# Optimization experiments

Measured on AMD Instinct MI355X. Metric: run time of the kernel, lower is better.

## Reference

```python
import jax, jax.numpy as jnp
import numpy as np
from jax import lax

SEGMENTS = 64
KERNEL = 5


def setup_inputs() -> dict:
    key = jax.random.key(0)
    k1, k2, k3 = jax.random.split(key, 3)
    B, S, F = 4, 4096, 1024
    A6 = 512 * 6
    inp = jax.random.normal(k1, (B, S, F), dtype=jnp.float32)
    W = jax.random.normal(k2, (A6, F), dtype=jnp.float32) * (1.0 / np.sqrt(F))
    b = jax.random.normal(k3, (A6,), dtype=jnp.float32) * 0.01
    return {"inp": inp, "W": W, "b": b}


def reference(inp, W, b):
    # Fused projection: [B,S,F] @ [F,6A] -> [B,S,6A]
    x = jnp.einsum('bsf,af->bsa', inp, W) + b
    qry, key, val, seg, loc, out = jnp.split(x, 6, axis=2)  # each [B,S,A]
    B, S, A = out.shape

    # Global aggregated attention branch
    agg = qry.mean(axis=1)                              # [B,A]
    scores = jnp.einsum('ba,bsa->bs', agg, key)         # [B,S]
    w = jax.nn.softmax(scores, axis=1)                  # [B,S]
    ctx = jnp.einsum('bs,bsa->ba', w, val)              # [B,A]
    aggregated = ctx[:, None, :] * out                  # [B,S,A]

    # Segment max-pool branch
    nseg = S // SEGMENTS
    seg4 = seg.reshape(B, nseg, SEGMENTS, A)
    seg_max = seg4.max(axis=2, keepdims=True)           # [B,nseg,1,A]
    segment_max_pooled = (seg_max * out.reshape(B, nseg, SEGMENTS, A)).reshape(B, S, A)

    # Local sliding-window max-pool branch (stride 1, pad KERNEL//2, -inf padding)
    pad = KERNEL // 2
    local_max_pooled = lax.reduce_window(
        loc, -jnp.inf, lax.max,
        window_dimensions=(1, KERNEL, 1),
        window_strides=(1, 1, 1),
        padding=((0, 0), (pad, pad), (0, 0)))           # [B,S,A]

    return aggregated + segment_max_pooled + local_max_pooled
```

## Files before the change

kernel.cpp:

```cpp
#include <hip/hip_runtime.h>
#include <hip/hip_bf16.h>
#include <stdint.h>

#define B_    4
#define S_    4096
#define F_    1024
#define A_    512
#define N3_   1536
#define M_    16384

#define BM    256
#define BK    64
#define NT    (F_ / BK)
#define LDP   266

typedef __attribute__((ext_vector_type(8))) __bf16 bf16x8;
typedef __attribute__((ext_vector_type(4))) float  f32x4;

__device__ __forceinline__ float bflo(unsigned int u) {
  union { unsigned int i; float f; } v; v.i = u << 16; return v.f;
}
__device__ __forceinline__ float bfhi(unsigned int u) {
  union { unsigned int i; float f; } v; v.i = u & 0xffff0000u; return v.f;
}
__device__ __forceinline__ float bf1(unsigned short u) {
  union { unsigned int i; float f; } v; v.i = ((unsigned int)u) << 16; return v.f;
}
__device__ __forceinline__ unsigned short bfc(float f) {
  return __builtin_bit_cast(unsigned short, __float2bfloat16(f));
}

__device__ __forceinline__ ushort4 cvt_bf4(float4 v) {
  ushort4 o;
  o.x = bfc(v.x); o.y = bfc(v.y); o.z = bfc(v.z); o.w = bfc(v.w);
  return o;
}

typedef __attribute__((address_space(3))) unsigned int lds_uint;
typedef const __attribute__((address_space(1))) unsigned int glob_uint;
__device__ __forceinline__ void lds_load16(const void* g, void* l) {
  __builtin_amdgcn_global_load_lds((glob_uint*)g, (lds_uint*)l, 16, 0, 0);
}

__global__ __launch_bounds__(256) void convert_mean_kernel(
    const float* __restrict__ inp, const float* __restrict__ W,
    unsigned short* __restrict__ inp_bf, unsigned short* __restrict__ w_bf,
    float* __restrict__ mu) {
  int blk = blockIdx.x;
  int t   = threadIdx.x;
  int r0  = blk * 32;
  int b   = r0 >> 12;
  float acc0 = 0.f, acc1 = 0.f, acc2 = 0.f, acc3 = 0.f;
  for (int r = 0; r < 32; r++) {
    size_t row = (size_t)(r0 + r);
    float4 v = ((const float4*)(inp + row * F_))[t];
    acc0 += v.x; acc1 += v.y; acc2 += v.z; acc3 += v.w;
    ((ushort4*)(inp_bf + row * F_))[t] = cvt_bf4(v);
  }
  atomicAdd(&mu[b * F_ + t * 4 + 0], acc0);
  atomicAdd(&mu[b * F_ + t * 4 + 1], acc1);
  atomicAdd(&mu[b * F_ + t * 4 + 2], acc2);
  atomicAdd(&mu[b * F_ + t * 4 + 3], acc3);

  const float* Wc = W + (size_t)N3_ * F_;
  const int n4 = (N3_ * F_) / 4;
  for (int i = blk * 256 + t; i < n4; i += 512 * 256) {
    ((ushort4*)w_bf)[i] = cvt_bf4(((const float4*)Wc)[i]);
  }
}

__global__ void agg_kernel(const float* __restrict__ mu, const float* __restrict__ W,
                           const float* __restrict__ bias, float* __restrict__ agg) {
  int gw = blockIdx.x * 4 + (threadIdx.x >> 6);
  int lane = threadIdx.x & 63;
  int b = gw >> 9, a = gw & 511;
  const float4* wr = (const float4*)(W + (size_t)a * F_);
  const float4* mr = (const float4*)(mu + b * F_);
  float s = 0.f;
#pragma unroll
  for (int k = 0; k < 4; k++) {
    float4 wv = wr[lane + 64 * k], mv = mr[lane + 64 * k];
    s += wv.x * mv.x + wv.y * mv.y + wv.z * mv.z + wv.w * mv.w;
  }
  for (int off = 32; off; off >>= 1) s += __shfl_down(s, off);
  if (lane == 0) agg[b * A_ + a] = s * (1.f / S_) + bias[a];
}

__global__ void v_kernel(const float* __restrict__ agg, const float* __restrict__ W,
                         const float* __restrict__ bias, float* __restrict__ v,
                         float* __restrict__ cvec) {
  int fc = blockIdx.x;
  int ac = blockIdx.y;
  int t = threadIdx.x;
  int f = fc * 256 + t;
  const float* Wk = W + (size_t)A_ * F_;
  float s0 = 0.f, s1 = 0.f, s2 = 0.f, s3 = 0.f;
  int a0 = ac * 64;
  for (int a = a0; a < a0 + 64; a++) {
    float wv = Wk[(size_t)a * F_ + f];
    s0 += agg[a] * wv;
    s1 += agg[A_ + a] * wv;
    s2 += agg[2 * A_ + a] * wv;
    s3 += agg[3 * A_ + a] * wv;
  }
  atomicAdd(&v[f], s0);
  atomicAdd(&v[F_ + f], s1);
  atomicAdd(&v[2 * F_ + f], s2);
  atomicAdd(&v[3 * F_ + f], s3);

  if (fc == 0 && ac == 0) {
    int bb = t >> 6, l = t & 63;
    float c = 0.f;
#pragma unroll
    for (int i = 0; i < 8; i++) c += agg[bb * A_ + l + 64 * i] * bias[A_ + l + 64 * i];
    for (int off = 32; off; off >>= 1) c += __shfl_down(c, off);
    if (l == 0) cvec[bb] = c;
  }
}

__global__ void scores_kernel(const unsigned short* __restrict__ inp_bf,
                              const float* __restrict__ v,
                              const float* __restrict__ cvec, float* __restrict__ scores) {
  int lane = threadIdx.x & 63;
  int row = blockIdx.x * 4 + (threadIdx.x >> 6);
  int b = row >> 12;
  const uint4* ip = (const uint4*)(inp_bf + (size_t)row * F_);
  const float4* vp = (const float4*)(v + b * F_);
  float s = 0.f;
#pragma unroll
  for (int k = 0; k < 2; k++) {
    uint4 x = ip[lane + 64 * k];
    float4 va = vp[(lane + 64 * k) * 2];
    float4 vb = vp[(lane + 64 * k) * 2 + 1];
    s += bflo(x.x) * va.x + bfhi(x.x) * va.y + bflo(x.y) * va.z + bfhi(x.y) * va.w +
         bflo(x.z) * vb.x + bfhi(x.z) * vb.y + bflo(x.w) * vb.z + bfhi(x.w) * vb.w;
  }
  for (int off = 32; off; off >>= 1) s += __shfl_down(s, off);
  if (lane == 0) scores[row] = s + cvec[b];
}

__global__ void softmax_kernel(float* __restrict__ sc) {
  __shared__ float red[256];
  int b = blockIdx.x, t = threadIdx.x;
  float* p = sc + b * S_;
  float vals[16];
  float m = -1e30f;
#pragma unroll
  for (int i = 0; i < 16; i++) { vals[i] = p[t + i * 256]; m = fmaxf(m, vals[i]); }
  red[t] = m; __syncthreads();
  for (int o = 128; o; o >>= 1) { if (t < o) red[t] = fmaxf(red[t], red[t + o]); __syncthreads(); }
  m = red[0]; __syncthreads();
  float sum = 0.f;
#pragma unroll
  for (int i = 0; i < 16; i++) { vals[i] = __expf(vals[i] - m); sum += vals[i]; }
  red[t] = sum; __syncthreads();
  for (int o = 128; o; o >>= 1) { if (t < o) red[t] += red[t + o]; __syncthreads(); }
  float inv = 1.f / red[0];
#pragma unroll
  for (int i = 0; i < 16; i++) p[t + i * 256] = vals[i] * inv;
}

__global__ void u_kernel(const unsigned short* __restrict__ inp_bf,
                         const float* __restrict__ w, float* __restrict__ u) {
  int b = blockIdx.z, fc = blockIdx.y, sc = blockIdx.x;
  int t = threadIdx.x;
  int f2 = fc * 512 + t * 2;
  int s0 = sc * 128;
  const float* wp = w + b * S_ + s0;
  const unsigned short* ip = inp_bf + ((size_t)(b * S_ + s0)) * F_ + f2;
  float a0 = 0.f, a1 = 0.f;
  for (int s = 0; s < 128; s++) {
    unsigned int xv = *(const unsigned int*)&ip[(size_t)s * F_];
    float ws = wp[s];
    a0 += ws * bflo(xv);
    a1 += ws * bfhi(xv);
  }
  atomicAdd(&u[b * F_ + f2], a0);
  atomicAdd(&u[b * F_ + f2 + 1], a1);
}

__global__ void ctx_kernel(const float* __restrict__ u, const float* __restrict__ W,
                           const float* __restrict__ bias, float* __restrict__ ctx) {
  int gw = blockIdx.x * 4 + (threadIdx.x >> 6);
  int lane = threadIdx.x & 63;
  int b = gw >> 9, a = gw & 511;
  const float4* wr = (const float4*)(W + (size_t)(2 * A_ + a) * F_);
  const float4* ur = (const float4*)(u + b * F_);
  float s = 0.f;
#pragma unroll
  for (int k = 0; k < 4; k++) {
    float4 wv = wr[lane + 64 * k], uv = ur[lane + 64 * k];
    s += wv.x * uv.x + wv.y * uv.y + wv.z * uv.z + wv.w * uv.w;
  }
  for (int off = 32; off; off >>= 1) s += __shfl_down(s, off);
  if (lane == 0) ctx[b * A_ + a] = s + bias[2 * A_ + a];
}

__global__ __launch_bounds__(512, 2) void gemm_fused(
    const __hip_bfloat16* __restrict__ Abf,
    const __hip_bfloat16* __restrict__ Wbf,
    const float* __restrict__ biasP,
    const float* __restrict__ ctx,
    float* __restrict__ out,
    unsigned short* __restrict__ sideLoc,
    float* __restrict__ sideGO) {
  extern __shared__ unsigned short smem[];
  unsigned short* ldsA = smem;
  unsigned short* ldsB = smem + 32768;
  unsigned short* Xt   = smem;
  float* segred = (float*)((char*)smem + 192 * LDP * 2);

  int bid = blockIdx.x;
  int swz = (bid & 7) * 64 + (bid >> 3);
  int mb = swz >> 3;
  int nb = swz & 7;

  int tid  = threadIdx.x;
  int lane = tid & 63;
  int wv   = tid >> 6;
  int wm   = wv >> 1;
  int wn   = wv & 1;
  int lo   = lane & 15, hi = lane >> 4, sw = lane & 7;

  int bir0 = (((hi * 16)      ^ (sw << 4)) >> 1);
  int bir1 = (((64 + hi * 16) ^ (sw << 4)) >> 1);

  const __hip_bfloat16* Ab = Abf + (size_t)mb * BM * F_;

  int srow = tid >> 3;
  int sel  = ((tid & 7) ^ (srow & 7)) * 8;
  int ldst = wv * 512;

  f32x4 acc[4][6];
#pragma unroll
  for (int i = 0; i < 4; i++)
#pragma unroll
    for (int j = 0; j < 6; j++) acc[i][j] = (f32x4){0.f, 0.f, 0.f, 0.f};

  int aBase = (wm * 64 + lo) * 64;
  int bBase = (wn * 96 + lo) * 64;

#define STG_A(kt_, buf_, r_)                                                              \
  lds_load16(Ab + (size_t)((r_) * 64 + srow) * F_ + (kt_) * BK + sel,                     \
             ldsA + (buf_) * 16384 + (r_) * 4096 + ldst)
#define STG_B(kt_, buf_, q_)                                                              \
  lds_load16(Wbf + (size_t)((q_) * 512 + nb * 64 + srow) * F_ + (kt_) * BK + sel,         \
             ldsB + (buf_) * 12288 + (q_) * 4096 + ldst)

  STG_A(0, 0, 0); STG_A(0, 0, 1); STG_A(0, 0, 2); STG_A(0, 0, 3);
  STG_B(0, 0, 0); STG_B(0, 0, 1); STG_B(0, 0, 2);

  for (int kt = 0; kt < NT; ++kt) {
    int c = kt & 1, nx = c ^ 1;
    bool pf = (kt + 1 < NT);
    const unsigned short* la = ldsA + c * 16384;
    const unsigned short* lb = ldsB + c * 12288;
    bf16x8 af[4][2], bfr[2][2];

    if (pf) {
      STG_A(kt + 1, nx, 0); STG_A(kt + 1, nx, 1); STG_A(kt + 1, nx, 2);
      asm volatile("s_waitcnt vmcnt(3)" ::: "memory");
    } else {
      asm volatile("s_waitcnt vmcnt(0)" ::: "memory");
    }
    __builtin_amdgcn_s_barrier();
#pragma unroll
    for (int i = 0; i < 4; i++) {
      af[i][0] = *(const bf16x8*)&la[aBase + i * 1024 + bir0];
      af[i][1] = *(const bf16x8*)&la[aBase + i * 1024 + bir1];
    }
#pragma unroll
    for (int j = 0; j < 2; j++) {
      bfr[j][0] = *(const bf16x8*)&lb[bBase + j * 1024 + bir0];
      bfr[j][1] = *(const bf16x8*)&lb[bBase + j * 1024 + bir1];
    }
    asm volatile("s_waitcnt lgkmcnt(0)" ::: "memory");
    __builtin_amdgcn_sched_barrier(0);
    __builtin_amdgcn_s_setprio(1);
#pragma unroll
    for (int i = 0; i < 4; i++)
#pragma unroll
      for (int j = 0; j < 2; j++) {
        acc[i][j] = __builtin_amdgcn_mfma_f32_16x16x32_bf16(af[i][0], bfr[j][0], acc[i][j], 0, 0, 0);
        acc[i][j] = __builtin_amdgcn_mfma_f32_16x16x32_bf16(af[i][1], bfr[j][1], acc[i][j], 0, 0, 0);
      }
    __builtin_amdgcn_s_setprio(0);
    __builtin_amdgcn_s_barrier();

#pragma unroll
    for (int j = 0; j < 2; j++) {
      bfr[j][0] = *(const bf16x8*)&lb[bBase + (2 + j) * 1024 + bir0];
      bfr[j][1] = *(const bf16x8*)&lb[bBase + (2 + j) * 1024 + bir1];
    }
    if (pf) { STG_A(kt + 1, nx, 3); STG_B(kt + 1, nx, 0); }
    __builtin_amdgcn_s_barrier();
    asm volatile("s_waitcnt lgkmcnt(0)" ::: "memory");
    __builtin_amdgcn_sched_barrier(0);
    __builtin_amdgcn_s_setprio(1);
#pragma unroll
    for (int i = 0; i < 4; i++)
#pragma unroll
      for (int j = 0; j < 2; j++) {
        acc[i][2 + j] = __builtin_amdgcn_mfma_f32_16x16x32_bf16(af[i][0], bfr[j][0], acc[i][2 + j], 0, 0, 0);
        acc[i][2 + j] = __builtin_amdgcn_mfma_f32_16x16x32_bf16(af[i][1], bfr[j][1], acc[i][2 + j], 0, 0, 0);
      }
    __builtin_amdgcn_s_setprio(0);
    __builtin_amdgcn_s_barrier();

#pragma unroll
    for (int j = 0; j < 2; j++) {
      bfr[j][0] = *(const bf16x8*)&lb[bBase + (4 + j) * 1024 + bir0];
      bfr[j][1] = *(const bf16x8*)&lb[bBase + (4 + j) * 1024 + bir1];
    }
    if (pf) { STG_B(kt + 1, nx, 1); STG_B(kt + 1, nx, 2); }
    __builtin_amdgcn_s_barrier();
    asm volatile("s_waitcnt lgkmcnt(0)" ::: "memory");
    __builtin_amdgcn_sched_barrier(0);
    __builtin_amdgcn_s_setprio(1);
#pragma unroll
    for (int i = 0; i < 4; i++)
#pragma unroll
      for (int j = 0; j < 2; j++) {
        acc[i][4 + j] = __builtin_amdgcn_mfma_f32_16x16x32_bf16(af[i][0], bfr[j][0], acc[i][4 + j], 0, 0, 0);
        acc[i][4 + j] = __builtin_amdgcn_mfma_f32_16x16x32_bf16(af[i][1], bfr[j][1], acc[i][4 + j], 0, 0, 0);
      }
    __builtin_amdgcn_s_setprio(0);
    __builtin_amdgcn_s_barrier();
  }
#undef STG_A
#undef STG_B

  float bias_r[6];
#pragma unroll
  for (int fj = 0; fj < 6; fj++) {
    int cl = wn * 96 + fj * 16 + lo;
    bias_r[fj] = biasP[(cl >> 6) * 512 + nb * 64 + (cl & 63)];
  }
#pragma unroll
  for (int fi = 0; fi < 4; fi++) {
#pragma unroll
    for (int fj = 0; fj < 6; fj++) {
      int cl = wn * 96 + fj * 16 + lo;
      int r  = wm * 64 + fi * 16 + hi * 4;
      float v0 = acc[fi][fj][0] + bias_r[fj];
      float v1 = acc[fi][fj][1] + bias_r[fj];
      float v2 = acc[fi][fj][2] + bias_r[fj];
      float v3 = acc[fi][fj][3] + bias_r[fj];
      unsigned int u01 = (unsigned int)bfc(v0) | ((unsigned int)bfc(v1) << 16);
      unsigned int u23 = (unsigned int)bfc(v2) | ((unsigned int)bfc(v3) << 16);
      *(unsigned int*)&Xt[cl * LDP + r]     = u01;
      *(unsigned int*)&Xt[cl * LDP + r + 2] = u23;
    }
  }
  __syncthreads();

  if (tid < 256) {
    int seg = tid >> 6, c = tid & 63;
    int base = c * LDP + seg * 64;
    float m = -1e30f;
#pragma unroll
    for (int k = 0; k < 32; k++) {
      unsigned int u = *(const unsigned int*)&Xt[base + 2 * k];
      m = fmaxf(m, fmaxf(bflo(u), bfhi(u)));
    }
    segred[seg * 64 + c] = m;
  }
  __syncthreads();

  {
    int c  = lane;
    int r0 = wv * 32;
    int b  = mb >> 4;
    int gcol = nb * 64 + c;
    float g = ctx[b * 512 + gcol] + segred[(r0 >> 6) * 64 + c];
    int lbase = (64 + c) * LDP;
    int obase = (128 + c) * LDP;
    float lw0 = bf1(Xt[lbase + max(r0 - 2, 0)]);
    float lw1 = bf1(Xt[lbase + max(r0 - 1, 0)]);
    float lw2 = bf1(Xt[lbase + r0]);
    float lw3 = bf1(Xt[lbase + r0 + 1]);
    size_t obase_g = ((size_t)(mb * 256 + r0)) * 512 + gcol;
#pragma unroll
    for (int j = 0; j < 32; j++) {
      int rn = min(r0 + j + 2, 255);
      float lw4 = bf1(Xt[lbase + rn]);
      float lm = fmaxf(fmaxf(fmaxf(lw0, lw1), fmaxf(lw2, lw3)), lw4);
      float o = bf1(Xt[obase + r0 + j]);
      out[obase_g + (size_t)j * 512] = g * o + lm;
      lw0 = lw1; lw1 = lw2; lw2 = lw3; lw3 = lw4;
    }
  }

  if (tid < 256) {
    int rsel = tid >> 6, c = tid & 63;
    int r = (rsel < 2) ? rsel : (252 + rsel);
    int b = mb >> 4;
    float g = ctx[b * 512 + nb * 64 + c] + segred[(r >> 6) * 64 + c];
    float o = bf1(Xt[(128 + c) * LDP + r]);
    int gr = mb * 4 + rsel;
    sideLoc[gr * 512 + nb * 64 + c] = Xt[(64 + c) * LDP + r];
    sideGO[gr * 512 + nb * 64 + c]  = g * o;
  }
}

__global__ void fixup_kernel(const unsigned short* __restrict__ sideLoc,
                             const float* __restrict__ sideGO,
                             float* __restrict__ out) {
  int rb = blockIdx.x;
  int tb = rb & 15;
  int t = threadIdx.x;
  int rsel = t >> 6, cq = t & 63;
#pragma unroll
  for (int k = 0; k < 8; k++) {
    int c = cq * 8 + k;
    float miss;
    int rl;
    if (rsel == 0) {
      if (tb == 0) continue;
      miss = fmaxf(bf1(sideLoc[((rb - 1) * 4 + 2) * 512 + c]),
                   bf1(sideLoc[((rb - 1) * 4 + 3) * 512 + c]));
      rl = 0;
    } else if (rsel == 1) {
      if (tb == 0) continue;
      miss = bf1(sideLoc[((rb - 1) * 4 + 3) * 512 + c]);
      rl = 1;
    } else if (rsel == 2) {
      if (tb == 15) continue;
      miss = bf1(sideLoc[((rb + 1) * 4 + 0) * 512 + c]);
      rl = 254;
    } else {
      if (tb == 15) continue;
      miss = fmaxf(bf1(sideLoc[((rb + 1) * 4 + 0) * 512 + c]),
                   bf1(sideLoc[((rb + 1) * 4 + 1) * 512 + c]));
      rl = 255;
    }
    size_t oi = ((size_t)rb * 256 + rl) * 512 + c;
    float cand = sideGO[(rb * 4 + rsel) * 512 + c] + miss;
    out[oi] = fmaxf(out[oi], cand);
  }
}

extern "C" void kernel_launch(void* const* d_in, const int* in_sizes, int n_in,
                              void* d_out, int out_size, void* d_ws, size_t ws_size,
                              hipStream_t stream) {
  const float* inp  = (const float*)d_in[0];
  const float* W    = (const float*)d_in[1];
  const float* bias = (const float*)d_in[2];
  float* out = (float*)d_out;
  char* ws = (char*)d_ws;

  const size_t INP_OFF  = 0;
  const size_t W_OFF    = 33554432;
  const size_t MU_OFF   = 36700160;
  const size_t U_OFF    = MU_OFF + 16384;
  const size_t V_OFF    = U_OFF + 16384;
  const size_t CV_OFF   = V_OFF + 16384;
  const size_t AGG_OFF  = CV_OFF + 256;
  const size_t CTX_OFF  = AGG_OFF + 8192;
  const size_t SC_OFF   = CTX_OFF + 8192;
  const size_t SL_OFF   = SC_OFF + 65536;
  const size_t SG_OFF   = SL_OFF + 262144;

  unsigned short* inp_bf = (unsigned short*)(ws + INP_OFF);
  unsigned short* w_bf   = (unsigned short*)(ws + W_OFF);
  float* mu     = (float*)(ws + MU_OFF);
  float* u      = (float*)(ws + U_OFF);
  float* v      = (float*)(ws + V_OFF);
  float* cvec   = (float*)(ws + CV_OFF);
  float* agg    = (float*)(ws + AGG_OFF);
  float* ctx    = (float*)(ws + CTX_OFF);
  float* scores = (float*)(ws + SC_OFF);
  unsigned short* sideLoc = (unsigned short*)(ws + SL_OFF);
  float* sideGO = (float*)(ws + SG_OFF);

  hipFuncSetAttribute(reinterpret_cast<const void*>(gemm_fused),
                      hipFuncAttributeMaxDynamicSharedMemorySize, 114688);

  hipMemsetAsync(ws + MU_OFF, 0, 3 * 16384 + 256, stream);
  convert_mean_kernel<<<512, 256, 0, stream>>>(inp, W, inp_bf, w_bf, mu);
  agg_kernel<<<512, 256, 0, stream>>>(mu, W, bias, agg);
  v_kernel<<<dim3(4, 8), 256, 0, stream>>>(agg, W, bias, v, cvec);
  scores_kernel<<<4096, 256, 0, stream>>>(inp_bf, v, cvec, scores);
  softmax_kernel<<<4, 256, 0, stream>>>(scores);
  u_kernel<<<dim3(32, 2, 4), 256, 0, stream>>>(inp_bf, scores, u);
  ctx_kernel<<<512, 256, 0, stream>>>(u, W, bias, ctx);
  gemm_fused<<<512, 512, 114688, stream>>>((const __hip_bfloat16*)inp_bf,
                                           (const __hip_bfloat16*)w_bf,
                                           bias + 3 * A_, ctx, out, sideLoc, sideGO);
  fixup_kernel<<<64, 256, 0, stream>>>(sideLoc, sideGO, out);
}
```

Before: 128.1 us.

## Merge attention chain into cooperative kernel and switch GEMM to 32x32 MFMA

Six small attention-chain kernels (agg, v, scores, softmax, u, ctx) are merged into one cooperative kernel that separates stages with grid-wide syncs, removing five launch gaps. The main fused GEMM moves from 16x16x32 to 32x32x16 bf16 MFMA tiles with a new swizzled LDS read pattern. Its K-loop is also restructured into two half-steps with fewer barriers and a reordered prefetch. Risks are grid.sync overhead and cooperative-launch residency limits, plus possible LDS bank conflicts from the new fragment layout.

```diff
diff --git a/kernel.cpp b/kernel.cpp
--- a/kernel.cpp
+++ b/kernel.cpp
@@ -1,6 +1,9 @@
 #include <hip/hip_runtime.h>
 #include <hip/hip_bf16.h>
+#include <hip/hip_cooperative_groups.h>
 #include <stdint.h>
+
+namespace cg = cooperative_groups;
 
 #define B_    4
 #define S_    4096
@@ -14,8 +17,11 @@
 #define NT    (F_ / BK)
 #define LDP   266
 
-typedef __attribute__((ext_vector_type(8))) __bf16 bf16x8;
-typedef __attribute__((ext_vector_type(4))) float  f32x4;
+typedef __attribute__((ext_vector_type(8)))  __bf16 bf16x8;
+typedef __attribute__((ext_vector_type(4)))  float  f32x4;
+typedef __attribute__((ext_vector_type(16))) float  f32x16;
+
+#define MFMA32(a, b, c) __builtin_amdgcn_mfma_f32_32x32x16_bf16((a), (b), (c), 0, 0, 0)
 
 __device__ __forceinline__ float bflo(unsigned int u) {
   union { unsigned int i; float f; } v; v.i = u << 16; return v.f;
@@ -29,7 +35,6 @@
 __device__ __forceinline__ unsigned short bfc(float f) {
   return __builtin_bit_cast(unsigned short, __float2bfloat16(f));
 }
-
 __device__ __forceinline__ ushort4 cvt_bf4(float4 v) {
   ushort4 o;
   o.x = bfc(v.x); o.y = bfc(v.y); o.z = bfc(v.z); o.w = bfc(v.w);
@@ -69,131 +74,134 @@
   }
 }
 
-__global__ void agg_kernel(const float* __restrict__ mu, const float* __restrict__ W,
-                           const float* __restrict__ bias, float* __restrict__ agg) {
-  int gw = blockIdx.x * 4 + (threadIdx.x >> 6);
-  int lane = threadIdx.x & 63;
-  int b = gw >> 9, a = gw & 511;
-  const float4* wr = (const float4*)(W + (size_t)a * F_);
-  const float4* mr = (const float4*)(mu + b * F_);
-  float s = 0.f;
-#pragma unroll
-  for (int k = 0; k < 4; k++) {
-    float4 wv = wr[lane + 64 * k], mv = mr[lane + 64 * k];
-    s += wv.x * mv.x + wv.y * mv.y + wv.z * mv.z + wv.w * mv.w;
-  }
-  for (int off = 32; off; off >>= 1) s += __shfl_down(s, off);
-  if (lane == 0) agg[b * A_ + a] = s * (1.f / S_) + bias[a];
-}
-
-__global__ void v_kernel(const float* __restrict__ agg, const float* __restrict__ W,
-                         const float* __restrict__ bias, float* __restrict__ v,
-                         float* __restrict__ cvec) {
-  int fc = blockIdx.x;
-  int ac = blockIdx.y;
-  int t = threadIdx.x;
-  int f = fc * 256 + t;
-  const float* Wk = W + (size_t)A_ * F_;
-  float s0 = 0.f, s1 = 0.f, s2 = 0.f, s3 = 0.f;
-  int a0 = ac * 64;
-  for (int a = a0; a < a0 + 64; a++) {
-    float wv = Wk[(size_t)a * F_ + f];
-    s0 += agg[a] * wv;
-    s1 += agg[A_ + a] * wv;
-    s2 += agg[2 * A_ + a] * wv;
-    s3 += agg[3 * A_ + a] * wv;
-  }
-  atomicAdd(&v[f], s0);
-  atomicAdd(&v[F_ + f], s1);
-  atomicAdd(&v[2 * F_ + f], s2);
-  atomicAdd(&v[3 * F_ + f], s3);
-
-  if (fc == 0 && ac == 0) {
-    int bb = t >> 6, l = t & 63;
-    float c = 0.f;
-#pragma unroll
-    for (int i = 0; i < 8; i++) c += agg[bb * A_ + l + 64 * i] * bias[A_ + l + 64 * i];
-    for (int off = 32; off; off >>= 1) c += __shfl_down(c, off);
-    if (l == 0) cvec[bb] = c;
-  }
-}
-
-__global__ void scores_kernel(const unsigned short* __restrict__ inp_bf,
-                              const float* __restrict__ v,
-                              const float* __restrict__ cvec, float* __restrict__ scores) {
-  int lane = threadIdx.x & 63;
-  int row = blockIdx.x * 4 + (threadIdx.x >> 6);
-  int b = row >> 12;
-  const uint4* ip = (const uint4*)(inp_bf + (size_t)row * F_);
-  const float4* vp = (const float4*)(v + b * F_);
-  float s = 0.f;
-#pragma unroll
-  for (int k = 0; k < 2; k++) {
-    uint4 x = ip[lane + 64 * k];
-    float4 va = vp[(lane + 64 * k) * 2];
-    float4 vb = vp[(lane + 64 * k) * 2 + 1];
-    s += bflo(x.x) * va.x + bfhi(x.x) * va.y + bflo(x.y) * va.z + bfhi(x.y) * va.w +
-         bflo(x.z) * vb.x + bfhi(x.z) * vb.y + bflo(x.w) * vb.z + bfhi(x.w) * vb.w;
-  }
-  for (int off = 32; off; off >>= 1) s += __shfl_down(s, off);
-  if (lane == 0) scores[row] = s + cvec[b];
-}
-
-__global__ void softmax_kernel(float* __restrict__ sc) {
-  __shared__ float red[256];
-  int b = blockIdx.x, t = threadIdx.x;
-  float* p = sc + b * S_;
-  float vals[16];
-  float m = -1e30f;
-#pragma unroll
-  for (int i = 0; i < 16; i++) { vals[i] = p[t + i * 256]; m = fmaxf(m, vals[i]); }
-  red[t] = m; __syncthreads();
-  for (int o = 128; o; o >>= 1) { if (t < o) red[t] = fmaxf(red[t], red[t + o]); __syncthreads(); }
-  m = red[0]; __syncthreads();
-  float sum = 0.f;
-#pragma unroll
-  for (int i = 0; i < 16; i++) { vals[i] = __expf(vals[i] - m); sum += vals[i]; }
-  red[t] = sum; __syncthreads();
-  for (int o = 128; o; o >>= 1) { if (t < o) red[t] += red[t + o]; __syncthreads(); }
-  float inv = 1.f / red[0];
-#pragma unroll
-  for (int i = 0; i < 16; i++) p[t + i * 256] = vals[i] * inv;
-}
-
-__global__ void u_kernel(const unsigned short* __restrict__ inp_bf,
-                         const float* __restrict__ w, float* __restrict__ u) {
-  int b = blockIdx.z, fc = blockIdx.y, sc = blockIdx.x;
-  int t = threadIdx.x;
-  int f2 = fc * 512 + t * 2;
-  int s0 = sc * 128;
-  const float* wp = w + b * S_ + s0;
-  const unsigned short* ip = inp_bf + ((size_t)(b * S_ + s0)) * F_ + f2;
-  float a0 = 0.f, a1 = 0.f;
-  for (int s = 0; s < 128; s++) {
-    unsigned int xv = *(const unsigned int*)&ip[(size_t)s * F_];
-    float ws = wp[s];
-    a0 += ws * bflo(xv);
-    a1 += ws * bfhi(xv);
-  }
-  atomicAdd(&u[b * F_ + f2], a0);
-  atomicAdd(&u[b * F_ + f2 + 1], a1);
-}
-
-__global__ void ctx_kernel(const float* __restrict__ u, const float* __restrict__ W,
-                           const float* __restrict__ bias, float* __restrict__ ctx) {
-  int gw = blockIdx.x * 4 + (threadIdx.x >> 6);
-  int lane = threadIdx.x & 63;
-  int b = gw >> 9, a = gw & 511;
-  const float4* wr = (const float4*)(W + (size_t)(2 * A_ + a) * F_);
-  const float4* ur = (const float4*)(u + b * F_);
-  float s = 0.f;
-#pragma unroll
-  for (int k = 0; k < 4; k++) {
-    float4 wv = wr[lane + 64 * k], uv = ur[lane + 64 * k];
-    s += wv.x * uv.x + wv.y * uv.y + wv.z * uv.z + wv.w * uv.w;
-  }
-  for (int off = 32; off; off >>= 1) s += __shfl_down(s, off);
-  if (lane == 0) ctx[b * A_ + a] = s + bias[2 * A_ + a];
+__global__ __launch_bounds__(512) void chain_kernel(
+    const float* __restrict__ mu, const float* __restrict__ W,
+    const float* __restrict__ bias, const unsigned short* __restrict__ inp_bf,
+    float* __restrict__ agg, float* __restrict__ v, float* __restrict__ cvec,
+    float* __restrict__ scores, float* __restrict__ u, float* __restrict__ ctx) {
+  cg::grid_group grid = cg::this_grid();
+  __shared__ float red[512];
+  int blk = blockIdx.x;
+  int t   = threadIdx.x;
+  int lane = t & 63, wv = t >> 6;
+
+  {
+    int gw = blk * 8 + wv;
+    int b = gw >> 9, a = gw & 511;
+    const float4* wr = (const float4*)(W + (size_t)a * F_);
+    const float4* mr = (const float4*)(mu + b * F_);
+    float s = 0.f;
+#pragma unroll
+    for (int k = 0; k < 4; k++) {
+      float4 wvv = wr[lane + 64 * k], mv = mr[lane + 64 * k];
+      s += wvv.x * mv.x + wvv.y * mv.y + wvv.z * mv.z + wvv.w * mv.w;
+    }
+    for (int off = 32; off; off >>= 1) s += __shfl_down(s, off);
+    if (lane == 0) agg[b * A_ + a] = s * (1.f / S_) + bias[a];
+  }
+  grid.sync();
+
+  {
+    int fc = blk & 1, ac = blk >> 1;
+    int f = fc * 512 + t;
+    const float* Wk = W + (size_t)A_ * F_;
+    float s0 = 0.f, s1 = 0.f, s2 = 0.f, s3 = 0.f;
+    int a0 = ac * 4;
+    for (int a = a0; a < a0 + 4; a++) {
+      float wvv = Wk[(size_t)a * F_ + f];
+      s0 += agg[a] * wvv;
+      s1 += agg[A_ + a] * wvv;
+      s2 += agg[2 * A_ + a] * wvv;
+      s3 += agg[3 * A_ + a] * wvv;
+    }
+    atomicAdd(&v[f], s0);
+    atomicAdd(&v[F_ + f], s1);
+    atomicAdd(&v[2 * F_ + f], s2);
+    atomicAdd(&v[3 * F_ + f], s3);
+    if (blk == 0 && wv < 4) {
+      float c = 0.f;
+#pragma unroll
+      for (int i = 0; i < 8; i++) c += agg[wv * A_ + lane + 64 * i] * bias[A_ + lane + 64 * i];
+      for (int off = 32; off; off >>= 1) c += __shfl_down(c, off);
+      if (lane == 0) cvec[wv] = c;
+    }
+  }
+  grid.sync();
+
+  {
+#pragma unroll
+    for (int d = 0; d < 8; d++) {
+      int row = blk * 64 + wv * 8 + d;
+      int b = row >> 12;
+      const uint4* ip = (const uint4*)(inp_bf + (size_t)row * F_);
+      const float4* vp = (const float4*)(v + b * F_);
+      float s = 0.f;
+#pragma unroll
+      for (int k = 0; k < 2; k++) {
+        uint4 x = ip[lane + 64 * k];
+        float4 va = vp[(lane + 64 * k) * 2];
+        float4 vb = vp[(lane + 64 * k) * 2 + 1];
+        s += bflo(x.x) * va.x + bfhi(x.x) * va.y + bflo(x.y) * va.z + bfhi(x.y) * va.w +
+             bflo(x.z) * vb.x + bfhi(x.z) * vb.y + bflo(x.w) * vb.z + bfhi(x.w) * vb.w;
+      }
+      for (int off = 32; off; off >>= 1) s += __shfl_down(s, off);
+      if (lane == 0) scores[row] = s + cvec[b];
+    }
+  }
+  grid.sync();
+
+  if (blk < 4) {
+    float* p = scores + blk * S_;
+    float vals[8];
+    float m = -1e30f;
+#pragma unroll
+    for (int i = 0; i < 8; i++) { vals[i] = p[t + i * 512]; m = fmaxf(m, vals[i]); }
+    red[t] = m; __syncthreads();
+    for (int o = 256; o; o >>= 1) { if (t < o) red[t] = fmaxf(red[t], red[t + o]); __syncthreads(); }
+    m = red[0]; __syncthreads();
+    float sum = 0.f;
+#pragma unroll
+    for (int i = 0; i < 8; i++) { vals[i] = __expf(vals[i] - m); sum += vals[i]; }
+    red[t] = sum; __syncthreads();
+    for (int o = 256; o; o >>= 1) { if (t < o) red[t] += red[t + o]; __syncthreads(); }
+    float inv = 1.f / red[0];
+#pragma unroll
+    for (int i = 0; i < 8; i++) p[t + i * 512] = vals[i] * inv;
+  }
+  grid.sync();
+
+  {
+    int b = blk & 3, sc = blk >> 2;
+    int s0 = sc * 64;
+    int f2 = t * 2;
+    const float* wp = scores + b * S_ + s0;
+    const unsigned short* ip = inp_bf + ((size_t)(b * S_ + s0)) * F_ + f2;
+    float a0 = 0.f, a1 = 0.f;
+    for (int s = 0; s < 64; s++) {
+      unsigned int xv = *(const unsigned int*)&ip[(size_t)s * F_];
+      float ws = wp[s];
+      a0 += ws * bflo(xv);
+      a1 += ws * bfhi(xv);
+    }
+    atomicAdd(&u[b * F_ + f2], a0);
+    atomicAdd(&u[b * F_ + f2 + 1], a1);
+  }
+  grid.sync();
+
+  {
+    int gw = blk * 8 + wv;
+    int b = gw >> 9, a = gw & 511;
+    const float4* wr = (const float4*)(W + (size_t)(2 * A_ + a) * F_);
+    const float4* ur = (const float4*)(u + b * F_);
+    float s = 0.f;
+#pragma unroll
+    for (int k = 0; k < 4; k++) {
+      float4 wvv = wr[lane + 64 * k], uv = ur[lane + 64 * k];
+      s += wvv.x * uv.x + wvv.y * uv.y + wvv.z * uv.z + wvv.w * uv.w;
+    }
+    for (int off = 32; off; off >>= 1) s += __shfl_down(s, off);
+    if (lane == 0) ctx[b * A_ + a] = s + bias[2 * A_ + a];
+  }
 }
 
 __global__ __launch_bounds__(512, 2) void gemm_fused(
@@ -220,10 +228,11 @@
   int wv   = tid >> 6;
   int wm   = wv >> 1;
   int wn   = wv & 1;
-  int lo   = lane & 15, hi = lane >> 4, sw = lane & 7;
-
-  int bir0 = (((hi * 16)      ^ (sw << 4)) >> 1);
-  int bir1 = (((64 + hi * 16) ^ (sw << 4)) >> 1);
+  int l31  = lane & 31, half = lane >> 5, r7 = l31 & 7;
+
+  int eo[4];
+#pragma unroll
+  for (int ks = 0; ks < 4; ks++) eo[ks] = ((ks * 2 + half) ^ r7) * 8;
 
   const __hip_bfloat16* Ab = Abf + (size_t)mb * BM * F_;
 
@@ -231,14 +240,15 @@
   int sel  = ((tid & 7) ^ (srow & 7)) * 8;
   int ldst = wv * 512;
 
-  f32x4 acc[4][6];
-#pragma unroll
-  for (int i = 0; i < 4; i++)
-#pragma unroll
-    for (int j = 0; j < 6; j++) acc[i][j] = (f32x4){0.f, 0.f, 0.f, 0.f};
-
-  int aBase = (wm * 64 + lo) * 64;
-  int bBase = (wn * 96 + lo) * 64;
+  const f32x16 zero16 = {0.f,0.f,0.f,0.f,0.f,0.f,0.f,0.f,0.f,0.f,0.f,0.f,0.f,0.f,0.f,0.f};
+  f32x16 acc[2][3];
+#pragma unroll
+  for (int i = 0; i < 2; i++)
+#pragma unroll
+    for (int j = 0; j < 3; j++) acc[i][j] = zero16;
+
+  int aRowBase = (wm * 64 + l31) * 64;
+  int bRowBase = (wn * 96 + l31) * 64;
 
 #define STG_A(kt_, buf_, r_)                                                              \
   lds_load16(Ab + (size_t)((r_) * 64 + srow) * F_ + (kt_) * BK + sel,                     \
@@ -255,101 +265,88 @@
     bool pf = (kt + 1 < NT);
     const unsigned short* la = ldsA + c * 16384;
     const unsigned short* lb = ldsB + c * 12288;
-    bf16x8 af[4][2], bfr[2][2];
-
+
+    __builtin_amdgcn_s_barrier();
     if (pf) {
-      STG_A(kt + 1, nx, 0); STG_A(kt + 1, nx, 1); STG_A(kt + 1, nx, 2);
-      asm volatile("s_waitcnt vmcnt(3)" ::: "memory");
+      STG_A(kt + 1, nx, 0); STG_A(kt + 1, nx, 1); STG_A(kt + 1, nx, 2); STG_A(kt + 1, nx, 3);
+      asm volatile("s_waitcnt vmcnt(4)" ::: "memory");
     } else {
       asm volatile("s_waitcnt vmcnt(0)" ::: "memory");
     }
     __builtin_amdgcn_s_barrier();
-#pragma unroll
-    for (int i = 0; i < 4; i++) {
-      af[i][0] = *(const bf16x8*)&la[aBase + i * 1024 + bir0];
-      af[i][1] = *(const bf16x8*)&la[aBase + i * 1024 + bir1];
-    }
-#pragma unroll
-    for (int j = 0; j < 2; j++) {
-      bfr[j][0] = *(const bf16x8*)&lb[bBase + j * 1024 + bir0];
-      bfr[j][1] = *(const bf16x8*)&lb[bBase + j * 1024 + bir1];
-    }
-    asm volatile("s_waitcnt lgkmcnt(0)" ::: "memory");
-    __builtin_amdgcn_sched_barrier(0);
+
+    bf16x8 a0[2][2], b0[3][2];
+#pragma unroll
+    for (int fi = 0; fi < 2; fi++)
+#pragma unroll
+      for (int ks = 0; ks < 2; ks++)
+        a0[fi][ks] = *(const bf16x8*)&la[aRowBase + fi * 2048 + eo[ks]];
+#pragma unroll
+    for (int fj = 0; fj < 3; fj++)
+#pragma unroll
+      for (int ks = 0; ks < 2; ks++)
+        b0[fj][ks] = *(const bf16x8*)&lb[bRowBase + fj * 2048 + eo[ks]];
     __builtin_amdgcn_s_setprio(1);
 #pragma unroll
-    for (int i = 0; i < 4; i++)
-#pragma unroll
-      for (int j = 0; j < 2; j++) {
-        acc[i][j] = __builtin_amdgcn_mfma_f32_16x16x32_bf16(af[i][0], bfr[j][0], acc[i][j], 0, 0, 0);
-        acc[i][j] = __builtin_amdgcn_mfma_f32_16x16x32_bf16(af[i][1], bfr[j][1], acc[i][j], 0, 0, 0);
-      }
+    for (int ks = 0; ks < 2; ks++)
+#pragma unroll
+      for (int fi = 0; fi < 2; fi++)
+#pragma unroll
+        for (int fj = 0; fj < 3; fj++)
+          acc[fi][fj] = MFMA32(a0[fi][ks], b0[fj][ks], acc[fi][fj]);
     __builtin_amdgcn_s_setprio(0);
-    __builtin_amdgcn_s_barrier();
-
-#pragma unroll
-    for (int j = 0; j < 2; j++) {
-      bfr[j][0] = *(const bf16x8*)&lb[bBase + (2 + j) * 1024 + bir0];
-      bfr[j][1] = *(const bf16x8*)&lb[bBase + (2 + j) * 1024 + bir1];
-    }
-    if (pf) { STG_A(kt + 1, nx, 3); STG_B(kt + 1, nx, 0); }
-    __builtin_amdgcn_s_barrier();
-    asm volatile("s_waitcnt lgkmcnt(0)" ::: "memory");
-    __builtin_amdgcn_sched_barrier(0);
+
+    if (pf) { STG_B(kt + 1, nx, 0); STG_B(kt + 1, nx, 1); STG_B(kt + 1, nx, 2); }
+
+#pragma unroll
+    for (int fi = 0; fi < 2; fi++)
+#pragma unroll
+      for (int ks = 0; ks < 2; ks++)
+        a0[fi][ks] = *(const bf16x8*)&la[aRowBase + fi * 2048 + eo[2 + ks]];
+#pragma unroll
+    for (int fj = 0; fj < 3; fj++)
+#pragma unroll
+      for (int ks = 0; ks < 2; ks++)
+        b0[fj][ks] = *(const bf16x8*)&lb[bRowBase + fj * 2048 + eo[2 + ks]];
     __builtin_amdgcn_s_setprio(1);
 #pragma unroll
-    for (int i = 0; i < 4; i++)
-#pragma unroll
-      for (int j = 0; j < 2; j++) {
-        acc[i][2 + j] = __builtin_amdgcn_mfma_f32_16x16x32_bf16(af[i][0], bfr[j][0], acc[i][2 + j], 0, 0, 0);
-        acc[i][2 + j] = __builtin_amdgcn_mfma_f32_16x16x32_bf16(af[i][1], bfr[j][1], acc[i][2 + j], 0, 0, 0);
-      }
+    for (int ks = 0; ks < 2; ks++)
+#pragma unroll
+      for (int fi = 0; fi < 2; fi++)
+#pragma unroll
+        for (int fj = 0; fj < 3; fj++)
+          acc[fi][fj] = MFMA32(a0[fi][ks], b0[fj][ks], acc[fi][fj]);
     __builtin_amdgcn_s_setprio(0);
-    __builtin_amdgcn_s_barrier();
-
-#pragma unroll
-    for (int j = 0; j < 2; j++) {
-      bfr[j][0] = *(const bf16x8*)&lb[bBase + (4 + j) * 1024 + bir0];
-      bfr[j][1] = *(const bf16x8*)&lb[bBase + (4 + j) * 1024 + bir1];
-    }
-    if (pf) { STG_B(kt + 1, nx, 1); STG_B(kt + 1, nx, 2); }
-    __builtin_amdgcn_s_barrier();
-    asm volatile("s_waitcnt lgkmcnt(0)" ::: "memory");
-    __builtin_amdgcn_sched_barrier(0);
-    __builtin_amdgcn_s_setprio(1);
-#pragma unroll
-    for (int i = 0; i < 4; i++)
-#pragma unroll
-      for (int j = 0; j < 2; j++) {
-        acc[i][4 + j] = __builtin_amdgcn_mfma_f32_16x16x32_bf16(af[i][0], bfr[j][0], acc[i][4 + j], 0, 0, 0);
-        acc[i][4 + j] = __builtin_amdgcn_mfma_f32_16x16x32_bf16(af[i][1], bfr[j][1], acc[i][4 + j], 0, 0, 0);
-      }
-    __builtin_amdgcn_s_setprio(0);
-    __builtin_amdgcn_s_barrier();
   }
 #undef STG_A
 #undef STG_B
 
-  float bias_r[6];
-#pragma unroll
-  for (int fj = 0; fj < 6; fj++) {
-    int cl = wn * 96 + fj * 16 + lo;
+  __syncthreads();
+
+  float bias_r[3];
+#pragma unroll
+  for (int fj = 0; fj < 3; fj++) {
+    int cl = wn * 96 + fj * 32 + l31;
     bias_r[fj] = biasP[(cl >> 6) * 512 + nb * 64 + (cl & 63)];
   }
 #pragma unroll
-  for (int fi = 0; fi < 4; fi++) {
-#pragma unroll
-    for (int fj = 0; fj < 6; fj++) {
-      int cl = wn * 96 + fj * 16 + lo;
-      int r  = wm * 64 + fi * 16 + hi * 4;
-      float v0 = acc[fi][fj][0] + bias_r[fj];
-      float v1 = acc[fi][fj][1] + bias_r[fj];
-      float v2 = acc[fi][fj][2] + bias_r[fj];
-      float v3 = acc[fi][fj][3] + bias_r[fj];
-      unsigned int u01 = (unsigned int)bfc(v0) | ((unsigned int)bfc(v1) << 16);
-      unsigned int u23 = (unsigned int)bfc(v2) | ((unsigned int)bfc(v3) << 16);
-      *(unsigned int*)&Xt[cl * LDP + r]     = u01;
-      *(unsigned int*)&Xt[cl * LDP + r + 2] = u23;
+  for (int fi = 0; fi < 2; fi++) {
+#pragma unroll
+    for (int fj = 0; fj < 3; fj++) {
+      int cl = wn * 96 + fj * 32 + l31;
+      int rbase = wm * 64 + fi * 32 + half * 4;
+#pragma unroll
+      for (int q = 0; q < 4; q++) {
+        int r = rbase + q * 8;
+        float v0 = acc[fi][fj][4 * q + 0] + bias_r[fj];
+        float v1 = acc[fi][fj][4 * q + 1] + bias_r[fj];
+        float v2 = acc[fi][fj][4 * q + 2] + bias_r[fj];
+        float v3 = acc[fi][fj][4 * q + 3] + bias_r[fj];
+        unsigned int u01 = (unsigned int)bfc(v0) | ((unsigned int)bfc(v1) << 16);
+        unsigned int u23 = (unsigned int)bfc(v2) | ((unsigned int)bfc(v3) << 16);
+        *(unsigned int*)&Xt[cl * LDP + r]     = u01;
+        *(unsigned int*)&Xt[cl * LDP + r + 2] = u23;
+      }
     }
   }
   __syncthreads();
@@ -360,8 +357,8 @@
     float m = -1e30f;
 #pragma unroll
     for (int k = 0; k < 32; k++) {
-      unsigned int u = *(const unsigned int*)&Xt[base + 2 * k];
-      m = fmaxf(m, fmaxf(bflo(u), bfhi(u)));
+      unsigned int uu = *(const unsigned int*)&Xt[base + 2 * k];
+      m = fmaxf(m, fmaxf(bflo(uu), bfhi(uu)));
     }
     segred[seg * 64 + c] = m;
   }
@@ -461,6 +458,7 @@
   const size_t SL_OFF   = SC_OFF + 65536;
   const size_t SG_OFF   = SL_OFF + 262144;
 
+  const unsigned short* inp_bf_c = (const unsigned short*)(ws + INP_OFF);
   unsigned short* inp_bf = (unsigned short*)(ws + INP_OFF);
   unsigned short* w_bf   = (unsigned short*)(ws + W_OFF);
   float* mu     = (float*)(ws + MU_OFF);
@@ -478,12 +476,12 @@
 
   hipMemsetAsync(ws + MU_OFF, 0, 3 * 16384 + 256, stream);
   convert_mean_kernel<<<512, 256, 0, stream>>>(inp, W, inp_bf, w_bf, mu);
-  agg_kernel<<<512, 256, 0, stream>>>(mu, W, bias, agg);
-  v_kernel<<<dim3(4, 8), 256, 0, stream>>>(agg, W, bias, v, cvec);
-  scores_kernel<<<4096, 256, 0, stream>>>(inp_bf, v, cvec, scores);
-  softmax_kernel<<<4, 256, 0, stream>>>(scores);
-  u_kernel<<<dim3(32, 2, 4), 256, 0, stream>>>(inp_bf, scores, u);
-  ctx_kernel<<<512, 256, 0, stream>>>(u, W, bias, ctx);
+
+  void* cargs[10] = {(void*)&mu, (void*)&W, (void*)&bias, (void*)&inp_bf_c,
+                     (void*)&agg, (void*)&v, (void*)&cvec, (void*)&scores,
+                     (void*)&u, (void*)&ctx};
+  hipLaunchCooperativeKernel((void*)chain_kernel, dim3(256), dim3(512), cargs, 0, stream);
+
   gemm_fused<<<512, 512, 114688, stream>>>((const __hip_bfloat16*)inp_bf,
                                            (const __hip_bfloat16*)w_bf,
                                            bias + 3 * A_, ctx, out, sideLoc, sideGO);
```

After: 264.1 us. +106.2%, slower.
